# Performance work log

Measured on AMD Instinct MI355X. Metric: run time of the kernel, lower is better.

Reference implementation:

```python
import jax, jax.numpy as jnp
import numpy as np

B, L, DC, DD, A = 32, 1024, 1024, 1024, 1024
NEG = -1e10


def setup_inputs() -> dict:
    key = jax.random.key(0)
    ks = jax.random.split(key, 16)
    s = lambda fan_in: 1.0 / np.sqrt(fan_in)
    return {
        "caption_features": jax.random.normal(ks[0], (B, L, DC), jnp.float32),
        "decoder_hidden": jax.random.normal(ks[1], (B, DD), jnp.float32),
        "word": jax.random.normal(ks[2], (B, DC), jnp.float32),
        "prev_caption_mask": jax.random.randint(ks[3], (B, L), 0, 2, jnp.int32),
        # cap_features_att: Linear(DC, A)
        "Wf": jax.random.uniform(ks[4], (A, DC), jnp.float32, -s(DC), s(DC)),
        "bf": jax.random.uniform(ks[5], (A,), jnp.float32, -s(DC), s(DC)),
        # cap_decoder_att: Linear(DD, A)
        "Wd": jax.random.uniform(ks[6], (A, DD), jnp.float32, -s(DD), s(DD)),
        "bd": jax.random.uniform(ks[7], (A,), jnp.float32, -s(DD), s(DD)),
        # cap_full_att: Linear(A, 1)
        "Wa": jax.random.uniform(ks[8], (1, A), jnp.float32, -s(A), s(A)),
        "ba": jax.random.uniform(ks[9], (1,), jnp.float32, -s(A), s(A)),
        # context_gate: Linear(2*DC + DD, DC)
        "Wg": jax.random.uniform(ks[10], (DC, 2 * DC + DD), jnp.float32, -s(2 * DC + DD), s(2 * DC + DD)),
        "bg": jax.random.uniform(ks[11], (DC,), jnp.float32, -s(2 * DC + DD), s(2 * DC + DD)),
        # sc_affine: Linear(DC, DC)
        "Ws": jax.random.uniform(ks[12], (DC, DC), jnp.float32, -s(DC), s(DC)),
        "bs": jax.random.uniform(ks[13], (DC,), jnp.float32, -s(DC), s(DC)),
        # tc_affine: Linear(2*DD, DC)
        "Wt": jax.random.uniform(ks[14], (DC, 2 * DD), jnp.float32, -s(2 * DD), s(2 * DD)),
        "bt": jax.random.uniform(ks[15], (DC,), jnp.float32, -s(2 * DD), s(2 * DD)),
    }


def reference(caption_features, decoder_hidden, word, prev_caption_mask,
              Wf, bf, Wd, bd, Wa, ba, Wg, bg, Ws, bs, Wt, bt):
    # additive (Bahdanau) attention scores: (B, L)
    att1 = jnp.einsum('bld,ad->bla', caption_features, Wf) + bf          # (B, L, A)
    att2 = decoder_hidden @ Wd.T + bd                                    # (B, A)
    scores = jnp.einsum('bla,a->bl', jnp.tanh(att1 + att2[:, None, :]), Wa[0]) + ba[0]
    scores = jnp.where(prev_caption_mask == 0, NEG, scores)
    alpha = jax.nn.softmax(scores, axis=1)                               # (B, L)
    context = jnp.einsum('bl,bld->bd', alpha, caption_features)          # (B, DC)
    # gated fusion
    zt = jax.nn.sigmoid(jnp.concatenate([word, decoder_hidden, context], axis=1) @ Wg.T + bg)
    sc = jnp.tanh(context @ Ws.T + bs)
    tc = jnp.tanh(jnp.concatenate([word, decoder_hidden], axis=1) @ Wt.T + bt)
    gated_context = zt * sc + (1.0 - zt) * tc
    return (gated_context, alpha)
```

## Files before the change

### kernel.cpp

```cpp
#include <hip/hip_runtime.h>
#include <hip/hip_bf16.h>
#include <cstdint>
#include <cstddef>

#define LOG2E 1.4426950408889634f

typedef __attribute__((ext_vector_type(8))) short short8;
typedef __attribute__((ext_vector_type(4))) float f32x4;

__device__ __forceinline__ float exp2f_fast(float x) { return __builtin_amdgcn_exp2f(x); }
__device__ __forceinline__ float rcp_fast(float x)   { return __builtin_amdgcn_rcpf(x); }
__device__ __forceinline__ float tanh_fast(float x) {
  float e = exp2f_fast(x * (2.0f * LOG2E));
  return 1.0f - 2.0f * rcp_fast(e + 1.0f);
}
__device__ __forceinline__ unsigned short f2b(float f) {
  union { float f; unsigned int u; } v; v.f = f;
  return (unsigned short)((v.u + 0x7FFFu + ((v.u >> 16) & 1u)) >> 16);
}
__device__ __forceinline__ float b2f(short h) {
  union { unsigned u; float f; } w; w.u = ((unsigned)(unsigned short)h) << 16;
  return w.f;
}

#define GLOAD_LDS16(g, l) \
  __builtin_amdgcn_global_load_lds((const __attribute__((address_space(1))) unsigned int*)(g), \
                                   (__attribute__((address_space(3))) unsigned int*)(l), 16, 0, 0)

__device__ __forceinline__ void skinny_gemm(
    const float* __restrict__ W, int Kfull,
    const float* __restrict__ x0, const float* __restrict__ x1,
    const float* __restrict__ x2,
    int kbeg, int kend, int n0, float* __restrict__ out)
{
  __shared__ unsigned char sX[4096];
  const int tid = threadIdx.x, lane = tid & 63, wv = tid >> 6;
  const int l15 = lane & 15, l4 = lane >> 4;
  f32x4 acc[2][2];
#pragma unroll
  for (int m = 0; m < 2; ++m)
#pragma unroll
    for (int j = 0; j < 2; ++j) acc[m][j] = (f32x4){0.f, 0.f, 0.f, 0.f};

  const int srow = tid >> 3, skc = (tid & 7) * 8;
  const int sbyte = srow * 128 + ((skc * 2) ^ ((srow & 7) << 4));

  for (int k0 = kbeg; k0 < kend; k0 += 64) {
    const float* xs = (k0 < 1024) ? x0 : (k0 < 2048) ? x1 : x2;
    const float* xp = xs + srow * 1024 + (k0 & 1023) + skc;
    float4 a = *reinterpret_cast<const float4*>(xp);
    float4 b = *reinterpret_cast<const float4*>(xp + 4);
    short8 h;
    h[0] = (short)f2b(a.x); h[1] = (short)f2b(a.y); h[2] = (short)f2b(a.z); h[3] = (short)f2b(a.w);
    h[4] = (short)f2b(b.x); h[5] = (short)f2b(b.y); h[6] = (short)f2b(b.z); h[7] = (short)f2b(b.w);
    *reinterpret_cast<short8*>(sX + sbyte) = h;
    __syncthreads();
#pragma unroll
    for (int ks = 0; ks < 2; ++ks) {
      short8 af[2], bfr[2];
#pragma unroll
      for (int m = 0; m < 2; ++m) {
        int r = m * 16 + l15;
        af[m] = *reinterpret_cast<const short8*>(
            sX + r * 128 + (((ks * 64) + l4 * 16) ^ ((r & 7) << 4)));
      }
#pragma unroll
      for (int j = 0; j < 2; ++j) {
        int n = n0 + wv * 32 + j * 16 + l15;
        const float* wp = W + (size_t)n * Kfull + k0 + ks * 32 + l4 * 8;
        float4 wa = *reinterpret_cast<const float4*>(wp);
        float4 wb = *reinterpret_cast<const float4*>(wp + 4);
        short8 hb;
        hb[0] = (short)f2b(wa.x); hb[1] = (short)f2b(wa.y); hb[2] = (short)f2b(wa.z); hb[3] = (short)f2b(wa.w);
        hb[4] = (short)f2b(wb.x); hb[5] = (short)f2b(wb.y); hb[6] = (short)f2b(wb.z); hb[7] = (short)f2b(wb.w);
        bfr[j] = hb;
      }
#pragma unroll
      for (int m = 0; m < 2; ++m)
#pragma unroll
        for (int j = 0; j < 2; ++j)
          acc[m][j] = __builtin_amdgcn_mfma_f32_16x16x32_bf16(af[m], bfr[j], acc[m][j], 0, 0, 0);
    }
    __syncthreads();
  }
#pragma unroll
  for (int m = 0; m < 2; ++m)
#pragma unroll
    for (int j = 0; j < 2; ++j)
#pragma unroll
      for (int r = 0; r < 4; ++r)
        atomicAdd(out + (size_t)(m * 16 + l4 * 4 + r) * 1024 + (n0 + wv * 32 + j * 16 + l15),
                  acc[m][j][r]);
}

__global__ __launch_bounds__(256) void convert_att2(
    const float* __restrict__ wf, unsigned short* __restrict__ wfb,
    const float* __restrict__ Wd, const float* __restrict__ dh,
    float* __restrict__ att2)
{
  const int bid = blockIdx.x;
  if (bid < 128) {
    const int base = bid * 1024;
#pragma unroll
    for (int j = 0; j < 4; ++j) {
      int g = base + j * 256 + (int)threadIdx.x;
      const float* s = wf + (size_t)g * 8;
      float4 a = *reinterpret_cast<const float4*>(s);
      float4 b = *reinterpret_cast<const float4*>(s + 4);
      short8 o;
      o[0] = (short)f2b(a.x); o[1] = (short)f2b(a.y); o[2] = (short)f2b(a.z); o[3] = (short)f2b(a.w);
      o[4] = (short)f2b(b.x); o[5] = (short)f2b(b.y); o[6] = (short)f2b(b.z); o[7] = (short)f2b(b.w);
      *reinterpret_cast<short8*>(wfb + (size_t)g * 8) = o;
    }
  } else {
    int bid2 = bid - 128;
    int nt = bid2 & 7, ks = bid2 >> 3;
    skinny_gemm(Wd, 1024, dh, dh, dh, ks * 256, ks * 256 + 256, nt * 128, att2);
  }
}

__global__ __launch_bounds__(256) void gate_gemm(
    const float* __restrict__ Wg, const float* __restrict__ Ws_,
    const float* __restrict__ Wt, const float* __restrict__ word,
    const float* __restrict__ dh, const float* __restrict__ ctx,
    float* __restrict__ ztp, float* __restrict__ scp, float* __restrict__ tcp)
{
  const int nt = blockIdx.x, slot = blockIdx.y;
  if (slot < 12)
    skinny_gemm(Wg, 3072, word, dh, ctx, slot * 256, slot * 256 + 256, nt * 128, ztp);
  else if (slot < 16)
    skinny_gemm(Ws_, 1024, ctx, ctx, ctx, (slot - 12) * 256, (slot - 12) * 256 + 256, nt * 128, scp);
  else
    skinny_gemm(Wt, 2048, word, dh, dh, (slot - 16) * 256, (slot - 16) * 256 + 256, nt * 128, tcp);
}

__global__ __launch_bounds__(512, 2) void att_gemm3(
    const float* __restrict__ cap, const unsigned short* __restrict__ wfb,
    const float* __restrict__ att2pre, const float* __restrict__ bfv,
    const float* __restrict__ bdv, const float* __restrict__ Wa,
    float* __restrict__ scores)
{
  __shared__ __align__(16) unsigned char lds[131072];
  const int tid = threadIdx.x, lane = tid & 63, wv = tid >> 6;
  const int j = ((int)blockIdx.x & 7) * 64 + ((int)blockIdx.x >> 3);
  const int mt = j >> 2, nt = j & 3;
  const int m0 = mt << 8, n0 = nt << 8;
  const int bb = m0 >> 10;
  const int wm = wv >> 2, wn = wv & 3;
  const int l15 = lane & 15, l4 = lane >> 4;
  const int r8 = lane >> 3, c8 = lane & 7;
  const unsigned swb = (unsigned)((l15 & 7) << 4);

  const float* capA = cap + (size_t)(m0 + wv * 32 + r8) * 1024 +
                      ((unsigned)((c8 * 16) ^ (r8 << 4)) >> 1);
  const unsigned char* bSrc = (const unsigned char*)wfb +
      (size_t)(n0 + wv * 32 + r8) * 2048 + ((c8 * 16) ^ (r8 << 4));
  const unsigned ldsBase = (unsigned)(size_t)(&lds[0]);

  f32x4 acc[8][4];
#pragma unroll
  for (int mf = 0; mf < 8; ++mf)
#pragma unroll
    for (int nf = 0; nf < 4; ++nf) acc[mf][nf] = (f32x4){0.f, 0.f, 0.f, 0.f};

#define STAGE_B(t) do { \
    const int sl__ = (t) & 1; \
    unsigned char* db__ = lds + sl__ * 65536 + 32768 + wv * 4096; \
    const unsigned char* gb__ = bSrc + (t) * 128; \
    GLOAD_LDS16(gb__,          db__); \
    GLOAD_LDS16(gb__ + 16384,  db__ + 1024); \
    GLOAD_LDS16(gb__ + 32768,  db__ + 2048); \
    GLOAD_LDS16(gb__ + 49152,  db__ + 3072); \
  } while (0)

#define FLIGHT(fA0, fA1, fB0, fB1, j0, tt) do { \
    const float* p0__ = capA + (size_t)(j0) * 8192 + (tt) * 64; \
    const float* p1__ = p0__ + 8192; \
    fA0 = *reinterpret_cast<const float4*>(p0__); \
    fA1 = *reinterpret_cast<const float4*>(p0__ + 4); \
    fB0 = *reinterpret_cast<const float4*>(p1__); \
    fB1 = *reinterpret_cast<const float4*>(p1__ + 4); \
  } while (0)

#define PACK_WRITE(fA, fB, wp) do { \
    short8 o__; \
    o__[0] = (short)f2b(fA.x); o__[1] = (short)f2b(fA.y); \
    o__[2] = (short)f2b(fA.z); o__[3] = (short)f2b(fA.w); \
    o__[4] = (short)f2b(fB.x); o__[5] = (short)f2b(fB.y); \
    o__[6] = (short)f2b(fB.z); o__[7] = (short)f2b(fB.w); \
    *reinterpret_cast<short8*>(wp) = o__; \
  } while (0)

#define DSREAD(dst, addr) \
  asm volatile("ds_read_b128 %0, %1" : "=v"(dst) : "v"(addr))

#define READ_AQ(dst, q) do { \
_Pragma("unroll") \
    for (int mf2 = 0; mf2 < 2; ++mf2) \
_Pragma("unroll") \
      for (int ks = 0; ks < 2; ++ks) { \
        unsigned r__ = (unsigned)(wm * 128 + (q) * 32 + mf2 * 16 + l15); \
        DSREAD(dst[mf2 * 2 + ks], sA + r__ * 128 + (((unsigned)(ks * 64 + l4 * 16)) ^ swb)); \
      } \
  } while (0)

#define READ_B(ch) do { \
_Pragma("unroll") \
    for (int nf = 0; nf < 2; ++nf) \
_Pragma("unroll") \
      for (int ks = 0; ks < 2; ++ks) { \
        unsigned c__ = (unsigned)(wn * 64 + (ch) * 32 + nf * 16 + l15); \
        DSREAD(Breg[(ch) * 4 + nf * 2 + ks], sB + c__ * 128 + (((unsigned)(ks * 64 + l4 * 16)) ^ swb)); \
      } \
  } while (0)

#define MFMA8(q, ch, Aq) do { \
    __builtin_amdgcn_s_setprio(1); \
_Pragma("unroll") \
    for (int mf2 = 0; mf2 < 2; ++mf2) \
_Pragma("unroll") \
      for (int nf = 0; nf < 2; ++nf) \
_Pragma("unroll") \
        for (int ks = 0; ks < 2; ++ks) \
          acc[(q) * 2 + mf2][(ch) * 2 + nf] = __builtin_amdgcn_mfma_f32_16x16x32_bf16( \
              Aq[mf2 * 2 + ks], Breg[(ch) * 4 + nf * 2 + ks], acc[(q) * 2 + mf2][(ch) * 2 + nf], 0, 0, 0); \
    __builtin_amdgcn_s_setprio(0); \
  } while (0)

#define WAIT_LGKM(n) do { \
    asm volatile("s_waitcnt lgkmcnt(" #n ")" ::: "memory"); \
    __builtin_amdgcn_sched_barrier(0); \
  } while (0)

  short8 Aq0[4], Aq1[4], Breg[8];
  float4 g0a, g0b, g1a, g1b;
  float4 g2a, g2b, g3a, g3b;

  STAGE_B(0);
  FLIGHT(g0a, g0b, g1a, g1b, 0, 0);
  FLIGHT(g2a, g2b, g3a, g3b, 2, 0);
  asm volatile("s_waitcnt vmcnt(0)" ::: "memory");
  {
    unsigned char* wp = lds + wv * 4096 + lane * 16;
    PACK_WRITE(g0a, g0b, wp);
    PACK_WRITE(g1a, g1b, wp + 1024);
    PACK_WRITE(g2a, g2b, wp + 2048);
    PACK_WRITE(g3a, g3b, wp + 3072);
  }
  FLIGHT(g0a, g0b, g1a, g1b, 0, 1);
  FLIGHT(g2a, g2b, g3a, g3b, 2, 1);
  WAIT_LGKM(0);
  asm volatile("s_barrier" ::: "memory");

  for (int t = 0; t < 16; ++t) {
    const unsigned sA = ldsBase + (unsigned)((t & 1) * 65536);
    const unsigned sB = sA + 32768u;

    if (t < 15) {
      asm volatile("s_waitcnt vmcnt(0)" ::: "memory");
      __builtin_amdgcn_sched_barrier(0);
      unsigned char* wp = lds + ((t + 1) & 1) * 65536 + wv * 4096 + lane * 16;
      PACK_WRITE(g0a, g0b, wp);
      PACK_WRITE(g1a, g1b, wp + 1024);
      PACK_WRITE(g2a, g2b, wp + 2048);
      PACK_WRITE(g3a, g3b, wp + 3072);
    }
    if (t < 15) STAGE_B(t + 1);

    READ_AQ(Aq0, 0);
    READ_B(0);
    READ_B(1);
    READ_AQ(Aq1, 1);

    WAIT_LGKM(8);
    MFMA8(0, 0, Aq0);
    WAIT_LGKM(4);
    MFMA8(0, 1, Aq0);
    WAIT_LGKM(0);
    READ_AQ(Aq0, 2);
    MFMA8(1, 0, Aq1);
    MFMA8(1, 1, Aq1);
    READ_AQ(Aq1, 3);
    WAIT_LGKM(4);
    MFMA8(2, 0, Aq0);
    MFMA8(2, 1, Aq0);
    if (t < 14) FLIGHT(g0a, g0b, g1a, g1b, 0, t + 2);
    WAIT_LGKM(0);
    MFMA8(3, 0, Aq1);
    MFMA8(3, 1, Aq1);
    if (t < 14) FLIGHT(g2a, g2b, g3a, g3b, 2, t + 2);

    if (t < 15) {
      if (t < 14) {
        asm volatile("s_waitcnt vmcnt(8)" ::: "memory");
      } else {
        asm volatile("s_waitcnt vmcnt(0)" ::: "memory");
      }
      asm volatile("s_barrier" ::: "memory");
    }
  }

  float colb[4], wav[4];
#pragma unroll
  for (int nf = 0; nf < 4; ++nf) {
    int cg = n0 + wn * 64 + nf * 16 + l15;
    colb[nf] = att2pre[bb * 1024 + cg] + bfv[cg] + bdv[cg];
    wav[nf]  = Wa[cg];
  }
#pragma unroll
  for (int mf = 0; mf < 8; ++mf) {
#pragma unroll
    for (int r = 0; r < 4; ++r) {
      float s = tanh_fast(acc[mf][0][r] + colb[0]) * wav[0]
              + tanh_fast(acc[mf][1][r] + colb[1]) * wav[1]
              + tanh_fast(acc[mf][2][r] + colb[2]) * wav[2]
              + tanh_fast(acc[mf][3][r] + colb[3]) * wav[3];
      s += __shfl_xor(s, 1);
      s += __shfl_xor(s, 2);
      s += __shfl_xor(s, 4);
      s += __shfl_xor(s, 8);
      if (l15 == 0)
        atomicAdd(scores + (m0 + wm * 128 + mf * 16 + l4 * 4 + r), s);
    }
  }
#undef STAGE_B
#undef FLIGHT
#undef PACK_WRITE
#undef DSREAD
#undef READ_AQ
#undef READ_B
#undef MFMA8
#undef WAIT_LGKM
}

__global__ __launch_bounds__(256) void softmax_k(
    const float* __restrict__ scores, const int* __restrict__ mask,
    float* __restrict__ alpha)
{
  const int b = blockIdx.x, tid = threadIdx.x;
  __shared__ float red[8];
  float s[4];
  float mx = -3.0e38f;
#pragma unroll
  for (int i = 0; i < 4; ++i) {
    int l = tid + i * 256;
    float v = scores[b * 1024 + l];
    v = (mask[b * 1024 + l] == 0) ? -1.0e10f : v;
    s[i] = v;
    mx = fmaxf(mx, v);
  }
  for (int off = 1; off < 64; off <<= 1) mx = fmaxf(mx, __shfl_xor(mx, off));
  int wv = tid >> 6;
  if ((tid & 63) == 0) red[wv] = mx;
  __syncthreads();
  mx = fmaxf(fmaxf(red[0], red[1]), fmaxf(red[2], red[3]));
  float sum = 0.f;
#pragma unroll
  for (int i = 0; i < 4; ++i) {
    s[i] = exp2f_fast((s[i] - mx) * LOG2E);
    sum += s[i];
  }
  for (int off = 1; off < 64; off <<= 1) sum += __shfl_xor(sum, off);
  if ((tid & 63) == 0) red[4 + wv] = sum;
  __syncthreads();
  sum = red[4] + red[5] + red[6] + red[7];
  float inv = 1.0f / sum;
#pragma unroll
  for (int i = 0; i < 4; ++i) alpha[b * 1024 + tid + i * 256] = s[i] * inv;
}

__global__ __launch_bounds__(256) void ctx_kb(
    const float* __restrict__ cap, const float* __restrict__ alpha,
    float* __restrict__ ctx)
{
  const int b = blockIdx.y, lc = blockIdx.x;
  const int dc = threadIdx.x & 127, loff = threadIdx.x >> 7;
  float acc[8] = {0.f, 0.f, 0.f, 0.f, 0.f, 0.f, 0.f, 0.f};
  for (int l = lc * 128 + loff; l < lc * 128 + 128; l += 2) {
    float av = alpha[b * 1024 + l];
    if (av != 0.f) {
      const float* p = cap + (((size_t)(b * 1024 + l)) << 10) + dc * 8;
      float4 v0 = *reinterpret_cast<const float4*>(p);
      float4 v1 = *reinterpret_cast<const float4*>(p + 4);
      acc[0] += av * v0.x; acc[1] += av * v0.y;
      acc[2] += av * v0.z; acc[3] += av * v0.w;
      acc[4] += av * v1.x; acc[5] += av * v1.y;
      acc[6] += av * v1.z; acc[7] += av * v1.w;
    }
  }
#pragma unroll
  for (int j = 0; j < 8; ++j) atomicAdd(ctx + b * 1024 + dc * 8 + j, acc[j]);
}

__global__ __launch_bounds__(256) void final_k(
    const float* __restrict__ ztp, const float* __restrict__ scp,
    const float* __restrict__ tcp, const float* __restrict__ bg,
    const float* __restrict__ bs, const float* __restrict__ bt,
    float* __restrict__ out)
{
  const int idx = blockIdx.x * 256 + threadIdx.x;
  const int d = idx & 1023;
  float z  = rcp_fast(1.0f + exp2f_fast(-(ztp[idx] + bg[d]) * LOG2E));
  float sc = tanh_fast(scp[idx] + bs[d]);
  float tc = tanh_fast(tcp[idx] + bt[d]);
  out[idx] = z * sc + (1.0f - z) * tc;
}

extern "C" void kernel_launch(void* const* d_in, const int* in_sizes, int n_in,
                              void* d_out, int out_size, void* d_ws, size_t ws_size,
                              hipStream_t stream) {
  const float* cap  = (const float*)d_in[0];
  const float* dh   = (const float*)d_in[1];
  const float* word = (const float*)d_in[2];
  const int*   mask = (const int*)d_in[3];
  const float* Wf   = (const float*)d_in[4];
  const float* bf   = (const float*)d_in[5];
  const float* Wd   = (const float*)d_in[6];
  const float* bd   = (const float*)d_in[7];
  const float* Wa   = (const float*)d_in[8];
  const float* Wg   = (const float*)d_in[10];
  const float* bg   = (const float*)d_in[11];
  const float* Ws   = (const float*)d_in[12];
  const float* bs   = (const float*)d_in[13];
  const float* Wt   = (const float*)d_in[14];
  const float* bt   = (const float*)d_in[15];

  float* out_g = (float*)d_out;
  float* alpha = (float*)d_out + 32768;

  float* att2pre = (float*)d_ws;
  float* scores  = att2pre + 32768;
  float* ctx     = scores + 32768;
  float* ztp     = ctx + 32768;
  float* scp     = ztp + 32768;
  float* tcp     = scp + 32768;
  unsigned short* wfb = (unsigned short*)((char*)d_ws + 786432);

  hipMemsetAsync(d_ws, 0, 6 * 32768 * sizeof(float), stream);

  convert_att2<<<160, 256, 0, stream>>>(Wf, wfb, Wd, dh, att2pre);
  att_gemm3<<<512, 512, 0, stream>>>(cap, wfb, att2pre, bf, bd, Wa, scores);
  softmax_k<<<32, 256, 0, stream>>>(scores, mask, alpha);
  ctx_kb<<<dim3(8, 32), 256, 0, stream>>>(cap, alpha, ctx);
  gate_gemm<<<dim3(8, 24), 256, 0, stream>>>(Wg, Ws, Wt, word, dh, ctx, ztp, scp, tcp);
  final_k<<<128, 256, 0, stream>>>(ztp, scp, tcp, bg, bs, bt, out_g);
}
```

Measured before the change: 144.0 us.

## Fuse softmax into context kernel and halve skinny GEMM K-splits

Merges the softmax and context-weighted-sum kernels into one launch. Each block recomputes the row softmax redundantly and then accumulates a 64-row chunk of caption features, which removes a launch and the alpha round trip. It also halves the K-slice size of the skinny GEMMs in convert_att2 and gate_gemm, doubling their grid to get more parallelism at the cost of more atomic adds. The redundant softmax work scales with the number of chunks per batch row.

Result: faster. 140.5 us (-2.5%).

```diff
diff --git a/kernel.cpp b/kernel.cpp
--- a/kernel.cpp
+++ b/kernel.cpp
@@ -115,7 +115,7 @@
   } else {
     int bid2 = bid - 128;
     int nt = bid2 & 7, ks = bid2 >> 3;
-    skinny_gemm(Wd, 1024, dh, dh, dh, ks * 256, ks * 256 + 256, nt * 128, att2);
+    skinny_gemm(Wd, 1024, dh, dh, dh, ks * 128, ks * 128 + 128, nt * 128, att2);
   }
 }
 
@@ -126,12 +126,12 @@
     float* __restrict__ ztp, float* __restrict__ scp, float* __restrict__ tcp)
 {
   const int nt = blockIdx.x, slot = blockIdx.y;
-  if (slot < 12)
-    skinny_gemm(Wg, 3072, word, dh, ctx, slot * 256, slot * 256 + 256, nt * 128, ztp);
-  else if (slot < 16)
-    skinny_gemm(Ws_, 1024, ctx, ctx, ctx, (slot - 12) * 256, (slot - 12) * 256 + 256, nt * 128, scp);
+  if (slot < 24)
+    skinny_gemm(Wg, 3072, word, dh, ctx, slot * 128, slot * 128 + 128, nt * 128, ztp);
+  else if (slot < 32)
+    skinny_gemm(Ws_, 1024, ctx, ctx, ctx, (slot - 24) * 128, (slot - 24) * 128 + 128, nt * 128, scp);
   else
-    skinny_gemm(Wt, 2048, word, dh, dh, (slot - 16) * 256, (slot - 16) * 256 + 256, nt * 128, tcp);
+    skinny_gemm(Wt, 2048, word, dh, dh, (slot - 32) * 128, (slot - 32) * 128 + 128, nt * 128, tcp);
 }
 
 __global__ __launch_bounds__(512, 2) void att_gemm3(
@@ -333,12 +333,14 @@
 #undef WAIT_LGKM
 }
 
-__global__ __launch_bounds__(256) void softmax_k(
+__global__ __launch_bounds__(256) void sm_ctx_k(
     const float* __restrict__ scores, const int* __restrict__ mask,
-    float* __restrict__ alpha)
-{
-  const int b = blockIdx.x, tid = threadIdx.x;
+    const float* __restrict__ cap, float* __restrict__ alpha,
+    float* __restrict__ ctx)
+{
+  const int b = blockIdx.y, lc = blockIdx.x, tid = threadIdx.x;
   __shared__ float red[8];
+  __shared__ float aChunk[64];
   float s[4];
   float mx = -3.0e38f;
 #pragma unroll
@@ -365,21 +367,21 @@
   __syncthreads();
   sum = red[4] + red[5] + red[6] + red[7];
   float inv = 1.0f / sum;
-#pragma unroll
-  for (int i = 0; i < 4; ++i) alpha[b * 1024 + tid + i * 256] = s[i] * inv;
-}
-
-__global__ __launch_bounds__(256) void ctx_kb(
-    const float* __restrict__ cap, const float* __restrict__ alpha,
-    float* __restrict__ ctx)
-{
-  const int b = blockIdx.y, lc = blockIdx.x;
-  const int dc = threadIdx.x & 127, loff = threadIdx.x >> 7;
+
+  const int i0 = lc >> 2, t0 = (lc & 3) * 64;
+  if ((unsigned)(tid - t0) < 64u) {
+    float av = s[i0] * inv;
+    alpha[b * 1024 + lc * 64 + (tid - t0)] = av;
+    aChunk[tid - t0] = av;
+  }
+  __syncthreads();
+
+  const int dc = tid & 127, loff = tid >> 7;
   float acc[8] = {0.f, 0.f, 0.f, 0.f, 0.f, 0.f, 0.f, 0.f};
-  for (int l = lc * 128 + loff; l < lc * 128 + 128; l += 2) {
-    float av = alpha[b * 1024 + l];
+  for (int li = loff; li < 64; li += 2) {
+    float av = aChunk[li];
     if (av != 0.f) {
-      const float* p = cap + (((size_t)(b * 1024 + l)) << 10) + dc * 8;
+      const float* p = cap + (((size_t)(b * 1024 + lc * 64 + li)) << 10) + dc * 8;
       float4 v0 = *reinterpret_cast<const float4*>(p);
       float4 v1 = *reinterpret_cast<const float4*>(p + 4);
       acc[0] += av * v0.x; acc[1] += av * v0.y;
@@ -438,10 +440,9 @@
 
   hipMemsetAsync(d_ws, 0, 6 * 32768 * sizeof(float), stream);
 
-  convert_att2<<<160, 256, 0, stream>>>(Wf, wfb, Wd, dh, att2pre);
+  convert_att2<<<192, 256, 0, stream>>>(Wf, wfb, Wd, dh, att2pre);
   att_gemm3<<<512, 512, 0, stream>>>(cap, wfb, att2pre, bf, bd, Wa, scores);
-  softmax_k<<<32, 256, 0, stream>>>(scores, mask, alpha);
-  ctx_kb<<<dim3(8, 32), 256, 0, stream>>>(cap, alpha, ctx);
-  gate_gemm<<<dim3(8, 24), 256, 0, stream>>>(Wg, Ws, Wt, word, dh, ctx, ztp, scp, tcp);
+  sm_ctx_k<<<dim3(16, 32), 256, 0, stream>>>(scores, mask, cap, alpha, ctx);
+  gate_gemm<<<dim3(8, 48), 256, 0, stream>>>(Wg, Ws, Wt, word, dh, ctx, ztp, scp, tcp);
   final_k<<<128, 256, 0, stream>>>(ztp, scp, tcp, bg, bs, bt, out_g);
 }
```
